# Kernel tuning notes

Measured on AMD Instinct MI355X. Metric: run time of the kernel, lower is better.

Reference implementation:

```python
import jax, jax.numpy as jnp
import numpy as np

B, T, E, H = 8, 2048, 1024, 64


def setup_inputs() -> dict:
    key = jax.random.key(0)
    kx, kq, kk, kv = jax.random.split(key, 4)
    x = jax.random.normal(kx, (B, T, E), dtype=jnp.float32)
    # nn.Linear(E, H, bias=False) weights, stored as (E, H) so y = x @ W
    scale = 0.02
    Wq = jax.random.normal(kq, (E, H), dtype=jnp.float32) * scale
    Wk = jax.random.normal(kk, (E, H), dtype=jnp.float32) * scale
    Wv = jax.random.normal(kv, (E, H), dtype=jnp.float32) * scale
    return {"x": x, "Wq": Wq, "Wk": Wk, "Wv": Wv}


def reference(x, Wq, Wk, Wv):
    # q, k, v: (B, T, H)
    q = x @ Wq
    k = x @ Wk
    v = x @ Wv
    # scores: (B, T, T)
    scores = jnp.einsum("btd,bsd->bts", q, k) / jnp.sqrt(jnp.asarray(H, q.dtype))
    # NOTE: the original module applies softmax over dim=0 (the batch dim).
    # With mask=None and is_decoder=False this is the only softmax applied.
    p = jax.nn.softmax(scores, axis=0)
    # output: (B, T, H)
    return jnp.einsum("bts,bsd->btd", p, v)
```

## Files before the change

### kernel.cpp

```cpp
#include <hip/hip_runtime.h>
#include <hip/hip_bf16.h>


typedef __attribute__((ext_vector_type(4))) float f32x4;
typedef __attribute__((ext_vector_type(4))) float float4_t;
typedef __attribute__((ext_vector_type(8))) short short8;
typedef __attribute__((ext_vector_type(4))) unsigned uint4_t;
typedef __attribute__((ext_vector_type(2))) unsigned uint2_t;

#define MFMA32(a, b, c) __builtin_amdgcn_mfma_f32_16x16x32_bf16(a, b, c, 0, 0, 0)

__device__ __forceinline__ short f2bf(float f) {
  unsigned u = __builtin_bit_cast(unsigned, f);
  unsigned r = (u + 0x7FFFu + ((u >> 16) & 1u)) >> 16;
  return (short)r;
}

__device__ __forceinline__ unsigned cvt_pk_bf16(float lo, float hi) {
  unsigned r;
  asm volatile("v_cvt_pk_bf16_f32 %0, %1, %2" : "=v"(r) : "v"(lo), "v"(hi));
  return r;
}

__device__ __forceinline__ void gload16(const short* g, short* l) {
  __builtin_amdgcn_global_load_lds(
      (const __attribute__((address_space(1))) unsigned*)g,
      (__attribute__((address_space(3))) unsigned*)l, 16, 0, 0);
}

__global__ __launch_bounds__(256) void wprep_kernel(
    const float* __restrict__ Wq, const float* __restrict__ Wk,
    const float* __restrict__ Wv, short* __restrict__ Wtb) {
  int lin = blockIdx.x * 256 + threadIdx.x;
  int n = lin & 63;
  int k8 = (lin >> 6) & 127;
  int wi = lin >> 13;
  const float* W = (wi == 0) ? Wq : (wi == 1) ? Wk : Wv;
  short* dst = Wtb + wi * 65536 + n * 1024 + k8 * 8;
#pragma unroll
  for (int i = 0; i < 8; i++) dst[i] = f2bf(W[(k8 * 8 + i) * 64 + n]);
}

__device__ __forceinline__ void proj_stage(const float* __restrict__ x,
                                           const short* __restrict__ Wtb,
                                           short* dst, int m0, int k0, int w, int l) {
  const int g = l >> 4, lr = l & 15;
#pragma unroll
  for (int i = 0; i < 10; i++) {
    int u = w * 10 + i;
    if (u < 16) {
      int wr = u >> 2, ks = (u >> 1) & 1, h = u & 1;
      const float* src = x + (size_t)(m0 + wr * 16 + lr) * 1024 + k0 + ks * 32 + g * 8 + h * 4;
      gload16((const short*)src, dst + u * 512);
    } else {
      int uu = u - 16, nf = uu >> 1, ks = uu & 1;
      const short* src = Wtb + (nf * 16 + lr) * 1024 + k0 + ks * 32 + g * 8;
      gload16(src, dst + u * 512);
    }
  }
}

__device__ __forceinline__ void proj_compute(const short* __restrict__ ldsb,
                                             f32x4 (&acc)[12], int w, int l) {
  short8 a[2];
#pragma unroll
  for (int ks = 0; ks < 2; ks++) {
    f32x4 fa = *(const f32x4*)&ldsb[(w * 4 + ks * 2 + 0) * 512 + l * 8];
    f32x4 fb = *(const f32x4*)&ldsb[(w * 4 + ks * 2 + 1) * 512 + l * 8];
    uint4_t u_;
    u_[0] = cvt_pk_bf16(fa[0], fa[1]);
    u_[1] = cvt_pk_bf16(fa[2], fa[3]);
    u_[2] = cvt_pk_bf16(fb[0], fb[1]);
    u_[3] = cvt_pk_bf16(fb[2], fb[3]);
    a[ks] = __builtin_bit_cast(short8, u_);
  }
#pragma unroll
  for (int nf = 0; nf < 12; nf++) {
#pragma unroll
    for (int ks = 0; ks < 2; ks++) {
      short8 bfrag = *(const short8*)&ldsb[(16 + nf * 2 + ks) * 512 + l * 8];
      acc[nf] = MFMA32(a[ks], bfrag, acc[nf]);
    }
  }
}

template <int I>
__device__ __forceinline__ void proj_step(const float* __restrict__ x,
                                          const short* __restrict__ Wtb, short* lds,
                                          f32x4 (&acc)[12], int m0, int w, int l) {
  constexpr int NW = (I == 15) ? 0 : 10;
  __builtin_amdgcn_sched_barrier(0);
  asm volatile("s_waitcnt vmcnt(%0) lgkmcnt(0)" ::"n"(NW) : "memory");
  __builtin_amdgcn_s_barrier();
  __builtin_amdgcn_sched_barrier(0);
  if constexpr (I + 2 < 16)
    proj_stage(x, Wtb, lds + ((I + 2) % 3) * 20480, m0, (I + 2) * 64, w, l);
  proj_compute(lds + (I % 3) * 20480, acc, w, l);
}

__global__ __launch_bounds__(256) void proj_kernel(
    const float* __restrict__ x, const short* __restrict__ Wtb,
    short* __restrict__ qb, short* __restrict__ kvb) {
  __shared__ __align__(16) short lds[3 * 40 * 512];
  const int tid = threadIdx.x;
  const int l = tid & 63, w = tid >> 6;
  const int g = l >> 4, lr = l & 15;
  const int m0 = blockIdx.x * 64;

  f32x4 acc[12];
#pragma unroll
  for (int i = 0; i < 12; i++) acc[i] = (f32x4){0.f, 0.f, 0.f, 0.f};

  proj_stage(x, Wtb, lds, m0, 0, w, l);
  proj_stage(x, Wtb, lds + 20480, m0, 64, w, l);

  proj_step<0>(x, Wtb, lds, acc, m0, w, l);
  proj_step<1>(x, Wtb, lds, acc, m0, w, l);
  proj_step<2>(x, Wtb, lds, acc, m0, w, l);
  proj_step<3>(x, Wtb, lds, acc, m0, w, l);
  proj_step<4>(x, Wtb, lds, acc, m0, w, l);
  proj_step<5>(x, Wtb, lds, acc, m0, w, l);
  proj_step<6>(x, Wtb, lds, acc, m0, w, l);
  proj_step<7>(x, Wtb, lds, acc, m0, w, l);
  proj_step<8>(x, Wtb, lds, acc, m0, w, l);
  proj_step<9>(x, Wtb, lds, acc, m0, w, l);
  proj_step<10>(x, Wtb, lds, acc, m0, w, l);
  proj_step<11>(x, Wtb, lds, acc, m0, w, l);
  proj_step<12>(x, Wtb, lds, acc, m0, w, l);
  proj_step<13>(x, Wtb, lds, acc, m0, w, l);
  proj_step<14>(x, Wtb, lds, acc, m0, w, l);
  proj_step<15>(x, Wtb, lds, acc, m0, w, l);

#pragma unroll
  for (int nf = 0; nf < 12; nf++) {
    int colg0 = nf * 16;
    int wi = colg0 >> 6;
    int d = (colg0 & 63) + lr;
    float scale = (wi == 0) ? 0.18033688f : 1.0f;
#pragma unroll
    for (int r = 0; r < 4; r++) {
      int row = m0 + w * 16 + g * 4 + r;
      int b = row >> 11, t = row & 2047;
      short bv = f2bf(acc[nf][r] * scale);
      if (wi == 0) {
        int idx = (((b * 128 + (t >> 4)) * 2 + (d >> 5)) * 64 +
                   ((((d >> 3) & 3) << 4) | (t & 15))) * 8 + (d & 7);
        qb[idx] = bv;
      } else if (wi == 1) {
        int u = (b << 2) | (((t >> 4) & 1) << 1) | (d >> 5);
        int idx = (((t >> 5) * 64 + u) << 9) +
                  ((((((d >> 3) & 3) << 4)) | (t & 15)) << 3) + (d & 7);
        kvb[idx] = bv;
      } else {
        int u = 32 + (b << 2) + (d >> 4);
        int idx = (((t >> 5) * 64 + u) << 9) +
                  (((((t >> 2) & 3) << 4) | (d & 15)) << 3) + (((t >> 4) & 1) << 2) + (t & 3);
        kvb[idx] = bv;
      }
    }
  }
}

__device__ __forceinline__ void stage_step(const short* __restrict__ kvb,
                                           short* lds_buf, int w, int l, int W) {
#pragma unroll
  for (int i = 0; i < 8; i++) {
    int u = w * 8 + i;
    const short* src = kvb + (((size_t)W * 64 + u) << 9) + l * 8;
    gload16(src, lds_buf + u * 512);
  }
}

__global__ __launch_bounds__(512, 2) void attn_kernel(
    const short* __restrict__ qb, const short* __restrict__ kvb,
    short* __restrict__ partial) {
  __shared__ __align__(16) short lds[2][64 * 512];
  const int tid = threadIdx.x;
  const int l = tid & 63, w = tid >> 6;
  const int tt = w >> 1, dh = w & 1;
  const int lin = blockIdx.x;
  const int sc = lin & 7;
  const int tblk = lin >> 3;
  const int tb16 = tblk * 4 + tt;

  short8 qf[8][2];
#pragma unroll
  for (int b = 0; b < 8; b++)
#pragma unroll
    for (int ks = 0; ks < 2; ks++)
      qf[b][ks] = *(const short8*)&qb[(size_t)((b * 128 + tb16) * 2 + ks) * 512 + l * 8];

  f32x4 oacc[8][2];
#pragma unroll
  for (int b = 0; b < 8; b++)
#pragma unroll
    for (int n = 0; n < 2; n++) oacc[b][n] = (f32x4){0.f, 0.f, 0.f, 0.f};

  stage_step(kvb, &lds[0][0], w, l, sc * 8);

  for (int it = 0; it < 8; it++) {
    __syncthreads();
    if (it + 1 < 8) stage_step(kvb, &lds[(it + 1) & 1][0], w, l, sc * 8 + it + 1);
    const short* ldsc = &lds[it & 1][0];

    uint2_t plo[8], phi[8];
#pragma unroll
    for (int sf = 0; sf < 2; sf++) {
      f32x4 S[8];
      __builtin_amdgcn_s_setprio(1);
#pragma unroll
      for (int b = 0; b < 8; b++) {
        short8 kf0 = *(const short8*)&ldsc[(b * 4 + sf * 2 + 0) * 512 + l * 8];
        short8 kf1 = *(const short8*)&ldsc[(b * 4 + sf * 2 + 1) * 512 + l * 8];
        f32x4 s = (f32x4){0.f, 0.f, 0.f, 0.f};
        s = MFMA32(kf0, qf[b][0], s);
        s = MFMA32(kf1, qf[b][1], s);
        S[b] = s;
      }
      __builtin_amdgcn_s_setprio(0);
#pragma unroll
      for (int r = 0; r < 4; r++) {
        float den = 0.f;
#pragma unroll
        for (int b = 0; b < 8; b++) {
          float e = __builtin_amdgcn_exp2f(S[b][r]);
          S[b][r] = e;
          den += e;
        }
        float inv = __builtin_amdgcn_rcpf(den);
#pragma unroll
        for (int b = 0; b < 8; b++) S[b][r] *= inv;
      }
#pragma unroll
      for (int b = 0; b < 8; b++) {
        uint2_t pw;
        pw[0] = cvt_pk_bf16(S[b][0], S[b][1]);
        pw[1] = cvt_pk_bf16(S[b][2], S[b][3]);
        if (sf == 0) plo[b] = pw; else phi[b] = pw;
      }
    }
    __builtin_amdgcn_s_setprio(1);
#pragma unroll
    for (int b = 0; b < 8; b++) {
      uint4_t pu;
      pu[0] = plo[b][0]; pu[1] = plo[b][1]; pu[2] = phi[b][0]; pu[3] = phi[b][1];
      short8 pbv = __builtin_bit_cast(short8, pu);
      short8 vf0 = *(const short8*)&ldsc[(32 + b * 4 + dh * 2 + 0) * 512 + l * 8];
      short8 vf1 = *(const short8*)&ldsc[(32 + b * 4 + dh * 2 + 1) * 512 + l * 8];
      oacc[b][0] = MFMA32(vf0, pbv, oacc[b][0]);
      oacc[b][1] = MFMA32(vf1, pbv, oacc[b][1]);
    }
    __builtin_amdgcn_s_setprio(0);
  }

  uint2_t* pout = (uint2_t*)partial;
#pragma unroll
  for (int b = 0; b < 8; b++)
#pragma unroll
    for (int n = 0; n < 2; n++) {
      int df = dh * 2 + n;
      uint2_t pk;
      pk[0] = cvt_pk_bf16(oacc[b][n][0], oacc[b][n][1]);
      pk[1] = cvt_pk_bf16(oacc[b][n][2], oacc[b][n][3]);
      __builtin_nontemporal_store(
          pk, &pout[(size_t)(((sc * 8 + b) * 128 + tb16) * 4 + df) * 64 + l]);
    }
}

__global__ __launch_bounds__(256) void reduce_kernel(const short* __restrict__ partial,
                                                     float* __restrict__ out) {
  int i = blockIdx.x * 256 + threadIdx.x;
  const uint2_t* p = (const uint2_t*)partial;
  float4_t a = (float4_t){0.f, 0.f, 0.f, 0.f};
  for (int sc = 0; sc < 8; sc++) {
    uint2_t v = __builtin_nontemporal_load(&p[(size_t)sc * 262144 + i]);
    a[0] += __builtin_bit_cast(float, v[0] << 16);
    a[1] += __builtin_bit_cast(float, v[0] & 0xFFFF0000u);
    a[2] += __builtin_bit_cast(float, v[1] << 16);
    a[3] += __builtin_bit_cast(float, v[1] & 0xFFFF0000u);
  }
  int b = i >> 15;
  int r1 = i & 32767;
  int tb16 = r1 >> 8;
  int r2 = r1 & 255;
  int df = r2 >> 6;
  int ll = r2 & 63;
  int gg = ll >> 4, lrr = ll & 15;
  *(float4_t*)&out[(size_t)(b * 2048 + tb16 * 16 + lrr) * 64 + df * 16 + gg * 4] = a;
}

extern "C" void kernel_launch(void* const* d_in, const int* in_sizes, int n_in,
                              void* d_out, int out_size, void* d_ws, size_t ws_size,
                              hipStream_t stream) {
  const float* x = (const float*)d_in[0];
  const float* Wq = (const float*)d_in[1];
  const float* Wk = (const float*)d_in[2];
  const float* Wv = (const float*)d_in[3];
  float* out = (float*)d_out;

  char* ws = (char*)d_ws;
  short* qb = (short*)ws;
  short* kvb = qb + 16384 * 64;
  short* partial = kvb + 2 * 16384 * 64;
  short* Wtb = partial + 8ull * 262144 * 4;

  wprep_kernel<<<96, 256, 0, stream>>>(Wq, Wk, Wv, Wtb);
  proj_kernel<<<256, 256, 0, stream>>>(x, Wtb, qb, kvb);
  attn_kernel<<<256, 512, 0, stream>>>(qb, kvb, partial);
  reduce_kernel<<<1024, 256, 0, stream>>>(partial, out);
}
```

Baseline: 62.67 us.

## Halve projection row tile, split warps 2x2, and double-buffer LDS

The projection GEMM now uses 32-row tiles over 512 blocks instead of 64-row tiles over 256. The four warps are arranged as 2 row groups by 2 column halves, so each warp keeps 6 accumulators instead of 12. The hand-unrolled triple-buffered pipeline with explicit waitcnt is replaced by a plain double-buffered loop using __syncthreads, and launch bounds request two blocks per CU. The aim is more occupancy and latency hiding on the memory-bound x stream. The cost is re-reading the bf16 weights twice as often and a shallower prefetch pipeline.

```diff
diff --git a/kernel.cpp b/kernel.cpp
--- a/kernel.cpp
+++ b/kernel.cpp
@@ -46,27 +46,28 @@
                                            short* dst, int m0, int k0, int w, int l) {
   const int g = l >> 4, lr = l & 15;
 #pragma unroll
-  for (int i = 0; i < 10; i++) {
-    int u = w * 10 + i;
-    if (u < 16) {
-      int wr = u >> 2, ks = (u >> 1) & 1, h = u & 1;
-      const float* src = x + (size_t)(m0 + wr * 16 + lr) * 1024 + k0 + ks * 32 + g * 8 + h * 4;
+  for (int i = 0; i < 8; i++) {
+    int u = w * 8 + i;
+    if (u < 8) {
+      int xwr = u >> 2, ks = (u >> 1) & 1, h = u & 1;
+      const float* src =
+          x + (size_t)(m0 + xwr * 16 + lr) * 1024 + k0 + ks * 32 + g * 8 + h * 4;
       gload16((const short*)src, dst + u * 512);
     } else {
-      int uu = u - 16, nf = uu >> 1, ks = uu & 1;
-      const short* src = Wtb + (nf * 16 + lr) * 1024 + k0 + ks * 32 + g * 8;
+      int uu = u - 8, cf = uu >> 1, ks = uu & 1;
+      const short* src = Wtb + (cf * 16 + lr) * 1024 + k0 + ks * 32 + g * 8;
       gload16(src, dst + u * 512);
     }
   }
 }
 
 __device__ __forceinline__ void proj_compute(const short* __restrict__ ldsb,
-                                             f32x4 (&acc)[12], int w, int l) {
+                                             f32x4 (&acc)[6], int wr, int wc, int l) {
   short8 a[2];
 #pragma unroll
   for (int ks = 0; ks < 2; ks++) {
-    f32x4 fa = *(const f32x4*)&ldsb[(w * 4 + ks * 2 + 0) * 512 + l * 8];
-    f32x4 fb = *(const f32x4*)&ldsb[(w * 4 + ks * 2 + 1) * 512 + l * 8];
+    f32x4 fa = *(const f32x4*)&ldsb[(wr * 4 + ks * 2 + 0) * 512 + l * 8];
+    f32x4 fb = *(const f32x4*)&ldsb[(wr * 4 + ks * 2 + 1) * 512 + l * 8];
     uint4_t u_;
     u_[0] = cvt_pk_bf16(fa[0], fa[1]);
     u_[1] = cvt_pk_bf16(fa[2], fa[3]);
@@ -75,71 +76,47 @@
     a[ks] = __builtin_bit_cast(short8, u_);
   }
 #pragma unroll
-  for (int nf = 0; nf < 12; nf++) {
+  for (int nf = 0; nf < 6; nf++) {
+    int cf = wc * 6 + nf;
 #pragma unroll
     for (int ks = 0; ks < 2; ks++) {
-      short8 bfrag = *(const short8*)&ldsb[(16 + nf * 2 + ks) * 512 + l * 8];
+      short8 bfrag = *(const short8*)&ldsb[(8 + cf * 2 + ks) * 512 + l * 8];
       acc[nf] = MFMA32(a[ks], bfrag, acc[nf]);
     }
   }
 }
 
-template <int I>
-__device__ __forceinline__ void proj_step(const float* __restrict__ x,
-                                          const short* __restrict__ Wtb, short* lds,
-                                          f32x4 (&acc)[12], int m0, int w, int l) {
-  constexpr int NW = (I == 15) ? 0 : 10;
-  __builtin_amdgcn_sched_barrier(0);
-  asm volatile("s_waitcnt vmcnt(%0) lgkmcnt(0)" ::"n"(NW) : "memory");
-  __builtin_amdgcn_s_barrier();
-  __builtin_amdgcn_sched_barrier(0);
-  if constexpr (I + 2 < 16)
-    proj_stage(x, Wtb, lds + ((I + 2) % 3) * 20480, m0, (I + 2) * 64, w, l);
-  proj_compute(lds + (I % 3) * 20480, acc, w, l);
-}
-
-__global__ __launch_bounds__(256) void proj_kernel(
+__global__ __launch_bounds__(256, 2) void proj_kernel(
     const float* __restrict__ x, const short* __restrict__ Wtb,
     short* __restrict__ qb, short* __restrict__ kvb) {
-  __shared__ __align__(16) short lds[3 * 40 * 512];
+  __shared__ __align__(16) short lds[2][32 * 512];
   const int tid = threadIdx.x;
   const int l = tid & 63, w = tid >> 6;
   const int g = l >> 4, lr = l & 15;
-  const int m0 = blockIdx.x * 64;
-
-  f32x4 acc[12];
-#pragma unroll
-  for (int i = 0; i < 12; i++) acc[i] = (f32x4){0.f, 0.f, 0.f, 0.f};
-
-  proj_stage(x, Wtb, lds, m0, 0, w, l);
-  proj_stage(x, Wtb, lds + 20480, m0, 64, w, l);
-
-  proj_step<0>(x, Wtb, lds, acc, m0, w, l);
-  proj_step<1>(x, Wtb, lds, acc, m0, w, l);
-  proj_step<2>(x, Wtb, lds, acc, m0, w, l);
-  proj_step<3>(x, Wtb, lds, acc, m0, w, l);
-  proj_step<4>(x, Wtb, lds, acc, m0, w, l);
-  proj_step<5>(x, Wtb, lds, acc, m0, w, l);
-  proj_step<6>(x, Wtb, lds, acc, m0, w, l);
-  proj_step<7>(x, Wtb, lds, acc, m0, w, l);
-  proj_step<8>(x, Wtb, lds, acc, m0, w, l);
-  proj_step<9>(x, Wtb, lds, acc, m0, w, l);
-  proj_step<10>(x, Wtb, lds, acc, m0, w, l);
-  proj_step<11>(x, Wtb, lds, acc, m0, w, l);
-  proj_step<12>(x, Wtb, lds, acc, m0, w, l);
-  proj_step<13>(x, Wtb, lds, acc, m0, w, l);
-  proj_step<14>(x, Wtb, lds, acc, m0, w, l);
-  proj_step<15>(x, Wtb, lds, acc, m0, w, l);
-
-#pragma unroll
-  for (int nf = 0; nf < 12; nf++) {
-    int colg0 = nf * 16;
+  const int wr = w & 1, wc = w >> 1;
+  const int m0 = blockIdx.x * 32;
+
+  f32x4 acc[6];
+#pragma unroll
+  for (int i = 0; i < 6; i++) acc[i] = (f32x4){0.f, 0.f, 0.f, 0.f};
+
+  proj_stage(x, Wtb, &lds[0][0], m0, 0, w, l);
+
+  for (int I = 0; I < 16; I++) {
+    __syncthreads();
+    if (I + 1 < 16) proj_stage(x, Wtb, &lds[(I + 1) & 1][0], m0, (I + 1) * 64, w, l);
+    proj_compute(&lds[I & 1][0], acc, wr, wc, l);
+  }
+
+#pragma unroll
+  for (int nf = 0; nf < 6; nf++) {
+    int colg0 = wc * 96 + nf * 16;
     int wi = colg0 >> 6;
     int d = (colg0 & 63) + lr;
     float scale = (wi == 0) ? 0.18033688f : 1.0f;
 #pragma unroll
     for (int r = 0; r < 4; r++) {
-      int row = m0 + w * 16 + g * 4 + r;
+      int row = m0 + wr * 16 + g * 4 + r;
       int b = row >> 11, t = row & 2047;
       short bv = f2bf(acc[nf][r] * scale);
       if (wi == 0) {
@@ -305,7 +282,7 @@
   short* Wtb = partial + 8ull * 262144 * 4;
 
   wprep_kernel<<<96, 256, 0, stream>>>(Wq, Wk, Wv, Wtb);
-  proj_kernel<<<256, 256, 0, stream>>>(x, Wtb, qb, kvb);
+  proj_kernel<<<512, 256, 0, stream>>>(x, Wtb, qb, kvb);
   attn_kernel<<<256, 512, 0, stream>>>(qb, kvb, partial);
   reduce_kernel<<<1024, 256, 0, stream>>>(partial, out);
 }
```

Result: slower. 73.55 us (+17.3%).
